# Performance work log

Measured on AMD Instinct MI355X. Metric: run time of the kernel, lower is better.

The kernel has to match this reference:

```python
import jax, jax.numpy as jnp
import numpy as np

H = 768
NH = 12
HD = H // NH
NDIM = 5
LN_EPS = 1e-5


def setup_inputs() -> dict:
    key = jax.random.key(0)
    ks = jax.random.split(key, 12)
    B, S = 4, 2048
    xavier = lambda k: jax.random.uniform(k, (H, H), jnp.float32, -1.0, 1.0) * np.sqrt(6.0 / (H + H))
    return {
        "hidden_states": jax.random.normal(ks[0], (B, S, H), jnp.float32),
        "Wq": xavier(ks[1]), "bq": jnp.zeros((H,), jnp.float32),
        "Wk": xavier(ks[2]), "bk": jnp.zeros((H,), jnp.float32),
        "Wv": xavier(ks[3]), "bv": jnp.zeros((H,), jnp.float32),
        "Wo": xavier(ks[4]), "bo": jnp.zeros((H,), jnp.float32),
        # per-dimension, per-head scalar biases (torch init: zeros; use small randn so grads are non-trivial)
        "dim_biases": 0.02 * jax.random.normal(ks[5], (NDIM, NH), jnp.float32),
        "ln_gamma": jnp.ones((H,), jnp.float32),
        "ln_beta": jnp.zeros((H,), jnp.float32),
        "attention_mask": jax.random.randint(ks[6], (4, 2048), 0, 2, jnp.int32),
        "dimension_idx": 2,
    }


def reference(hidden_states, Wq, bq, Wk, bk, Wv, bv, Wo, bo, dim_biases,
              ln_gamma, ln_beta, attention_mask, dimension_idx):
    B, S, _ = hidden_states.shape
    residual = hidden_states
    # torch nn.Linear: x @ W.T + b
    q = (hidden_states @ Wq.T + bq).reshape(B, S, NH, HD).transpose(0, 2, 1, 3)  # [B,NH,S,HD]
    k = (hidden_states @ Wk.T + bk).reshape(B, S, NH, HD).transpose(0, 2, 1, 3)
    v = (hidden_states @ Wv.T + bv).reshape(B, S, NH, HD).transpose(0, 2, 1, 3)

    scores = jnp.einsum("bhqd,bhkd->bhqk", q, k) / np.sqrt(HD)  # [B,NH,S,S]
    if dimension_idx is not None and dimension_idx < NDIM:
        scores = scores + dim_biases[dimension_idx][None, :, None, None]
    # mask over key positions, broadcast over heads and queries
    scores = jnp.where(attention_mask[:, None, None, :] == 0, -jnp.inf, scores)
    attn = jax.nn.softmax(scores, axis=-1)

    ctx = jnp.einsum("bhqk,bhkd->bhqd", attn, v)  # [B,NH,S,HD]
    ctx = ctx.transpose(0, 2, 1, 3).reshape(B, S, H)
    out = ctx @ Wo.T + bo

    y = out + residual
    mu = jnp.mean(y, axis=-1, keepdims=True)
    var = jnp.var(y, axis=-1, keepdims=True)
    y = (y - mu) / jnp.sqrt(var + LN_EPS) * ln_gamma + ln_beta
    return y
```

## Files before the change

### kernel.cpp

```cpp
#include <hip/hip_runtime.h>
#include <hip/hip_bf16.h>

#define HH    768
#define NHEAD 12
#define HDIM  64
#define BB    4
#define SS    2048
#define MM    (BB*SS)
#define NDIMS 5
#define WEL   (HH*HH)
#define LOG2E 1.44269504088896f
#define QSCALE 0.180336881f

typedef unsigned short u16;
typedef __attribute__((ext_vector_type(8))) short short8;
typedef __attribute__((ext_vector_type(4))) float floatx4;
typedef __attribute__((ext_vector_type(16))) float floatx16;
typedef __attribute__((ext_vector_type(4))) unsigned int uint4v;
typedef __attribute__((ext_vector_type(2))) unsigned int uint2v;

__device__ __forceinline__ float bf2f(u16 u) {
    return __uint_as_float(((unsigned int)u) << 16);
}
__device__ __forceinline__ u16 f2bf(float f) {
    unsigned int x = __float_as_uint(f);
    unsigned int r = (x + 0x7fffu + ((x >> 16) & 1u)) >> 16;
    return (u16)r;
}
__device__ __forceinline__ unsigned int pack_bf16x2(float a, float b) {
    float2 f2 = make_float2(a, b);
    __hip_bfloat162 h2 = __float22bfloat162_rn(f2);
    return *reinterpret_cast<unsigned int*>(&h2);
}
__device__ __forceinline__ void gld16(const u16* g, u16* l) {
    __builtin_amdgcn_global_load_lds(
        (const __attribute__((address_space(1))) unsigned int*)g,
        (__attribute__((address_space(3))) unsigned int*)l, 16, 0, 0);
}

__global__ __launch_bounds__(256) void f32_to_bf16(
    const float* __restrict__ in, u16* __restrict__ out, int n8)
{
    int i = blockIdx.x * 256 + threadIdx.x;
    if (i >= n8) return;
    float4 a = ((const float4*)in)[i*2];
    float4 b = ((const float4*)in)[i*2 + 1];
    ushort4 lo, hi;
    lo.x = f2bf(a.x); lo.y = f2bf(a.y); lo.z = f2bf(a.z); lo.w = f2bf(a.w);
    hi.x = f2bf(b.x); hi.y = f2bf(b.y); hi.z = f2bf(b.z); hi.w = f2bf(b.w);
    ((ushort4*)out)[i*2]     = lo;
    ((ushort4*)out)[i*2 + 1] = hi;
}

__global__ __launch_bounds__(256) void w_cvt4(
    const float* __restrict__ W0, const float* __restrict__ W1,
    const float* __restrict__ W2, const float* __restrict__ W3,
    u16* __restrict__ out)
{
    const float* src = (blockIdx.y == 0) ? W0 : (blockIdx.y == 1) ? W1
                     : (blockIdx.y == 2) ? W2 : W3;
    u16* dst = out + (size_t)blockIdx.y * WEL;
    int i = blockIdx.x * 256 + threadIdx.x;
    float4 a = ((const float4*)src)[i*2];
    float4 b = ((const float4*)src)[i*2 + 1];
    ushort4 lo, hi;
    lo.x = f2bf(a.x); lo.y = f2bf(a.y); lo.z = f2bf(a.z); lo.w = f2bf(a.w);
    hi.x = f2bf(b.x); hi.y = f2bf(b.y); hi.z = f2bf(b.z); hi.w = f2bf(b.w);
    ((ushort4*)dst)[i*2]     = lo;
    ((ushort4*)dst)[i*2 + 1] = hi;
}

__device__ __forceinline__ void gemm_gld_body(
    const u16* __restrict__ Xb, const u16* __restrict__ Wrows,
    const float* __restrict__ biasL, u16* __restrict__ outL, int i0)
{
    __shared__ u16 Xs[128][64];
    __shared__ u16 Ws[128][64];
    const int t = threadIdx.x;
    const int w = t >> 6, lane = t & 63;
    const int wy = w >> 1, wx = w & 1;
    const int m = lane & 31, hh = lane >> 5;

    const int grow = lane >> 3;
    const int cg   = (lane & 7) ^ grow;

    floatx16 acc[2][2];
    #pragma unroll
    for (int am = 0; am < 2; ++am)
        #pragma unroll
        for (int bn = 0; bn < 2; ++bn)
            #pragma unroll
            for (int r = 0; r < 16; ++r) acc[am][bn][r] = 0.f;

    for (int k0 = 0; k0 < HH; k0 += 64) {
        __syncthreads();
        #pragma unroll
        for (int j = 0; j < 4; ++j) {
            const int r = w*32 + j*8;
            gld16(Xb    + (size_t)(i0 + r + grow)*HH + k0 + cg*8, &Xs[r][0]);
            gld16(Wrows + (size_t)(r + grow)*HH      + k0 + cg*8, &Ws[r][0]);
        }
        __syncthreads();

        #pragma unroll
        for (int kh = 0; kh < 4; ++kh) {
            const int ch = kh*2 + hh;
            short8 af[2], bf[2];
            #pragma unroll
            for (int am = 0; am < 2; ++am) {
                const int row = wy*64 + am*32 + m;
                af[am] = *(const short8*)&Xs[row][(ch ^ (m & 7))*8];
            }
            #pragma unroll
            for (int bn = 0; bn < 2; ++bn) {
                const int row = wx*64 + bn*32 + m;
                bf[bn] = *(const short8*)&Ws[row][(ch ^ (m & 7))*8];
            }
            #pragma unroll
            for (int am = 0; am < 2; ++am)
                #pragma unroll
                for (int bn = 0; bn < 2; ++bn)
                    acc[am][bn] = __builtin_amdgcn_mfma_f32_32x32x16_bf16(
                        af[am], bf[bn], acc[am][bn], 0, 0, 0);
        }
    }

    float bb[2];
    #pragma unroll
    for (int bn = 0; bn < 2; ++bn) bb[bn] = biasL[wx*64 + bn*32 + m];
    #pragma unroll
    for (int am = 0; am < 2; ++am)
        #pragma unroll
        for (int bn = 0; bn < 2; ++bn)
            #pragma unroll
            for (int r = 0; r < 16; ++r) {
                int row = i0 + wy*64 + am*32 + (r & 3) + 8*(r >> 2) + 4*hh;
                outL[(size_t)row*HH + wx*64 + bn*32 + m] = f2bf(acc[am][bn][r] + bb[bn]);
            }
}

__global__ __launch_bounds__(256) void gemm_gld_qkv(
    const u16* __restrict__ Xb, const u16* __restrict__ Wb3,
    const float* __restrict__ bq, const float* __restrict__ bk, const float* __restrict__ bv,
    u16* __restrict__ oq, u16* __restrict__ ok, u16* __restrict__ ov)
{
    const int j0 = blockIdx.x * 128;
    const int sel = j0 / HH;
    const int lj = j0 - sel * HH;
    const float* bias = (sel == 0) ? bq : (sel == 1) ? bk : bv;
    u16* out = (sel == 0) ? oq : (sel == 1) ? ok : ov;
    gemm_gld_body(Xb, Wb3 + (size_t)j0 * HH, bias + lj, out + lj, blockIdx.y * 128);
}

__global__ __launch_bounds__(256) void gemm_gld_single(
    const u16* __restrict__ Xb, const u16* __restrict__ Wb,
    const float* __restrict__ bias, u16* __restrict__ out)
{
    const int j0 = blockIdx.x * 128;
    gemm_gld_body(Xb, Wb + (size_t)j0 * HH, bias + j0, out + j0, blockIdx.y * 128);
}

__global__ __launch_bounds__(256) void gemm_mfma_nt(
    const u16* __restrict__ Xb, const float* __restrict__ W,
    const float* __restrict__ bias, u16* __restrict__ out)
{
    __shared__ u16 Xs[128][40];
    __shared__ u16 Wt[64][40];
    const int t = threadIdx.x;
    const int w = t >> 6, lane = t & 63;
    const int c = lane & 15, qd = lane >> 4;
    const int i0 = blockIdx.y * 128, j0 = blockIdx.x * 64;
    const int xrow = t >> 1, xoff = (t & 1) * 16;
    const int wn = t >> 2, woff = (t & 3) * 8;

    floatx4 acc[2][4];
    #pragma unroll
    for (int mt = 0; mt < 2; ++mt)
        #pragma unroll
        for (int nt = 0; nt < 4; ++nt) acc[mt][nt] = (floatx4){0.f,0.f,0.f,0.f};

    for (int k0 = 0; k0 < HH; k0 += 32) {
        uint4 xa  = *(const uint4*)(Xb + (size_t)(i0 + xrow)*HH + k0 + xoff);
        uint4 xb2 = *(const uint4*)(Xb + (size_t)(i0 + xrow)*HH + k0 + xoff + 8);
        float4 wa = *(const float4*)(W + (size_t)(j0 + wn)*HH + k0 + woff);
        float4 wb = *(const float4*)(W + (size_t)(j0 + wn)*HH + k0 + woff + 4);
        __syncthreads();
        *(uint4*)&Xs[xrow][xoff]     = xa;
        *(uint4*)&Xs[xrow][xoff + 8] = xb2;
        ushort4 w0, w1;
        w0.x = f2bf(wa.x); w0.y = f2bf(wa.y); w0.z = f2bf(wa.z); w0.w = f2bf(wa.w);
        w1.x = f2bf(wb.x); w1.y = f2bf(wb.y); w1.z = f2bf(wb.z); w1.w = f2bf(wb.w);
        *(ushort4*)&Wt[wn][woff]     = w0;
        *(ushort4*)&Wt[wn][woff + 4] = w1;
        __syncthreads();

        short8 a0 = *(const short8*)&Xs[w*32 + c][qd*8];
        short8 a1 = *(const short8*)&Xs[w*32 + 16 + c][qd*8];
        #pragma unroll
        for (int nt = 0; nt < 4; ++nt) {
            short8 bfr = *(const short8*)&Wt[nt*16 + c][qd*8];
            acc[0][nt] = __builtin_amdgcn_mfma_f32_16x16x32_bf16(a0, bfr, acc[0][nt], 0, 0, 0);
            acc[1][nt] = __builtin_amdgcn_mfma_f32_16x16x32_bf16(a1, bfr, acc[1][nt], 0, 0, 0);
        }
    }

    float bv[4];
    #pragma unroll
    for (int nt = 0; nt < 4; ++nt) bv[nt] = bias[j0 + nt*16 + c];
    #pragma unroll
    for (int mt = 0; mt < 2; ++mt)
        #pragma unroll
        for (int nt = 0; nt < 4; ++nt)
            #pragma unroll
            for (int r = 0; r < 4; ++r)
                out[(size_t)(i0 + w*32 + mt*16 + qd*4 + r)*HH + j0 + nt*16 + c] =
                    f2bf(acc[mt][nt][r] + bv[nt]);
}

__global__ __launch_bounds__(256, 3) void attn_mfma32(
    const u16* __restrict__ Q, const u16* __restrict__ K, const u16* __restrict__ V,
    const float* __restrict__ dim_biases, const int* __restrict__ mask,
    const int* __restrict__ dim_idx_p, u16* __restrict__ ctx)
{
    __shared__ u16 Ks[2][64][64];
    __shared__ u16 Vt[2][64][64];
    __shared__ float madd[2][64];

    const int t = threadIdx.x;
    const int w = t >> 6, lane = t & 63;
    const int ql = lane & 31, hi = lane >> 5;
    const int sw7 = ql & 7;

    const int flat = blockIdx.x + 16 * (blockIdx.y + 12 * blockIdx.z);
    const int swz  = (flat & 7) * 96 + (flat >> 3);
    const int q0 = (swz & 15) * 128;
    const int h  = (swz >> 4) % NHEAD;
    const int b  = swz / (16 * NHEAD);

    const int didx = *dim_idx_p;
    const float db2 = ((didx < NDIMS) ? dim_biases[didx*NHEAD + h] : 0.f) * LOG2E;

    const int grow = lane >> 3;
    const int cg   = (lane & 7) ^ grow;
    const int vkp = t & 31;
    const int vdg = (t >> 5) * 8;

    short8 ones;
    #pragma unroll
    for (int j = 0; j < 8; ++j) ones[j] = (short)0x3F80;

    short8 qv[4];
    {
        const u16* qsrc = Q + ((size_t)(b*SS + q0 + w*32 + ql))*HH + h*HDIM + 8*hi;
        #pragma unroll
        for (int s = 0; s < 4; ++s) {
            ushort4 u0 = *(const ushort4*)(qsrc + s*16);
            ushort4 u1 = *(const ushort4*)(qsrc + s*16 + 4);
            const u16 uu[8] = {u0.x,u0.y,u0.z,u0.w,u1.x,u1.y,u1.z,u1.w};
            #pragma unroll
            for (int j = 0; j < 8; ++j)
                qv[s][j] = (short)f2bf(bf2f(uu[j]) * QSCALE);
        }
    }

    floatx16 o[2], lacc;
    #pragma unroll
    for (int r = 0; r < 16; ++r) { o[0][r] = 0.f; o[1][r] = 0.f; lacc[r] = 0.f; }

    auto stage = [&](int kt, int buf) {
        #pragma unroll
        for (int j = 0; j < 2; ++j) {
            const int rbase = w*16 + j*8;
            gld16(K + (size_t)(b*SS + kt*64 + rbase + grow)*HH + h*HDIM + cg*8,
                  &Ks[buf][rbase][0]);
        }
        const u16* va = V + ((size_t)(b*SS + kt*64 + 2*vkp))*HH + h*HDIM + vdg;
        const u16* vb = va + HH;
        ushort4 a0 = *(const ushort4*)va;
        ushort4 a1 = *(const ushort4*)(va + 4);
        ushort4 b0 = *(const ushort4*)vb;
        ushort4 b1 = *(const ushort4*)(vb + 4);
        const u16 aa[8] = {a0.x,a0.y,a0.z,a0.w,a1.x,a1.y,a1.z,a1.w};
        const u16 bb[8] = {b0.x,b0.y,b0.z,b0.w,b1.x,b1.y,b1.z,b1.w};
        #pragma unroll
        for (int i = 0; i < 8; ++i) {
            const int d = vdg + i;
            const int sc = (vkp >> 2) ^ (d & 7);
            *(unsigned int*)&Vt[buf][d][sc*8 + (vkp & 3)*2] =
                (unsigned int)aa[i] | ((unsigned int)bb[i] << 16);
        }
        if (t < 64)
            madd[buf][t] = (mask[(size_t)b*SS + kt*64 + t] != 0) ? db2 : -1e30f;
    };

    stage(0, 0);

    for (int kt = 0; kt < SS/64; ++kt) {
        const int cur = kt & 1;
        __syncthreads();
        if (kt + 1 < SS/64) stage(kt + 1, cur ^ 1);

        #pragma unroll
        for (int kblk = 0; kblk < 2; ++kblk) {
            const int krow = kblk*32 + ql;
            const u16* kb = &Ks[cur][krow][0];

            floatx16 z;
            #pragma unroll
            for (int qq = 0; qq < 4; ++qq) {
                float4 mv = *(const float4*)&madd[cur][kblk*32 + qq*8 + 4*hi];
                z[qq*4+0] = mv.x; z[qq*4+1] = mv.y; z[qq*4+2] = mv.z; z[qq*4+3] = mv.w;
            }
            #pragma unroll
            for (int s = 0; s < 4; ++s) {
                short8 kf = *(const short8*)(kb + ((s*2 + hi) ^ sw7)*8);
                z = __builtin_amdgcn_mfma_f32_32x32x16_bf16(kf, qv[s], z, 0, 0, 0);
            }
            #pragma unroll
            for (int r = 0; r < 16; ++r) z[r] = __builtin_amdgcn_exp2f(z[r]);

            #pragma unroll
            for (int ks = 0; ks < 2; ++ks) {
                unsigned x0 = pack_bf16x2(z[ks*8 + 0], z[ks*8 + 1]);
                unsigned y0 = pack_bf16x2(z[ks*8 + 4], z[ks*8 + 5]);
                unsigned x1 = pack_bf16x2(z[ks*8 + 2], z[ks*8 + 3]);
                unsigned y1 = pack_bf16x2(z[ks*8 + 6], z[ks*8 + 7]);
                uint2v s0 = __builtin_amdgcn_permlane32_swap(x0, y0, false, false);
                uint2v s1 = __builtin_amdgcn_permlane32_swap(x1, y1, false, false);
                uint4v pv; pv[0] = s0[0]; pv[1] = s1[0]; pv[2] = s0[1]; pv[3] = s1[1];
                short8 pa = __builtin_bit_cast(short8, pv);

                lacc = __builtin_amdgcn_mfma_f32_32x32x16_bf16(pa, ones, lacc, 0, 0, 0);
                const int ck = kblk*4 + ks*2 + hi;
                #pragma unroll
                for (int dblk = 0; dblk < 2; ++dblk) {
                    const int d = dblk*32 + ql;
                    short8 vf = *(const short8*)&Vt[cur][d][(ck ^ sw7)*8];
                    o[dblk] = __builtin_amdgcn_mfma_f32_32x32x16_bf16(pa, vf, o[dblk], 0, 0, 0);
                }
            }
        }
    }

    #pragma unroll
    for (int r = 0; r < 16; ++r) {
        float l = lacc[r];
        float inv = (l > 0.f) ? 1.f / l : 0.f;
        const int qrow = q0 + w*32 + (r & 3) + 8*(r >> 2) + 4*hi;
        u16* dst = ctx + ((size_t)(b*SS + qrow))*HH + h*HDIM + ql;
        dst[0]  = f2bf(o[0][r] * inv);
        dst[32] = f2bf(o[1][r] * inv);
    }
}

__global__ __launch_bounds__(256) void add_ln_wave(
    const u16* __restrict__ proj, const float* __restrict__ resid,
    const float* __restrict__ gamma, const float* __restrict__ beta,
    float* __restrict__ out)
{
    const int t = threadIdx.x, w = t >> 6, lane = t & 63;
    const int row = blockIdx.x * 4 + w;
    const size_t base = (size_t)row * HH + lane * 12;
    const int gbase = lane * 12;

    float x[12];
    #pragma unroll
    for (int j = 0; j < 3; ++j) {
        ushort4 p = *(const ushort4*)(proj + base + j*4);
        float4  r = *(const float4*)(resid + base + j*4);
        x[j*4+0] = bf2f(p.x) + r.x;
        x[j*4+1] = bf2f(p.y) + r.y;
        x[j*4+2] = bf2f(p.z) + r.z;
        x[j*4+3] = bf2f(p.w) + r.w;
    }
    float s = 0.f, ss = 0.f;
    #pragma unroll
    for (int j = 0; j < 12; ++j) { s += x[j]; ss += x[j]*x[j]; }
    #pragma unroll
    for (int off = 1; off < 64; off <<= 1) {
        s  += __shfl_xor(s, off);
        ss += __shfl_xor(ss, off);
    }
    float mean = s * (1.f/768.f);
    float var  = ss * (1.f/768.f) - mean*mean;
    float rstd = rsqrtf(fmaxf(var, 0.f) + 1e-5f);
    #pragma unroll
    for (int j = 0; j < 3; ++j) {
        float4 g = *(const float4*)(gamma + gbase + j*4);
        float4 bt = *(const float4*)(beta + gbase + j*4);
        float4 y;
        y.x = (x[j*4+0]-mean)*rstd*g.x + bt.x;
        y.y = (x[j*4+1]-mean)*rstd*g.y + bt.y;
        y.z = (x[j*4+2]-mean)*rstd*g.z + bt.z;
        y.w = (x[j*4+3]-mean)*rstd*g.w + bt.w;
        *(float4*)(out + base + j*4) = y;
    }
}

extern "C" void kernel_launch(void* const* d_in, const int* in_sizes, int n_in,
                              void* d_out, int out_size, void* d_ws, size_t ws_size,
                              hipStream_t stream)
{
    (void)in_sizes; (void)n_in; (void)out_size;
    const float* x    = (const float*)d_in[0];
    const float* Wq   = (const float*)d_in[1];
    const float* bq   = (const float*)d_in[2];
    const float* Wk   = (const float*)d_in[3];
    const float* bk   = (const float*)d_in[4];
    const float* Wv   = (const float*)d_in[5];
    const float* bv   = (const float*)d_in[6];
    const float* Wo   = (const float*)d_in[7];
    const float* bo   = (const float*)d_in[8];
    const float* dimb = (const float*)d_in[9];
    const float* gam  = (const float*)d_in[10];
    const float* bet  = (const float*)d_in[11];
    const int* mask   = (const int*)d_in[12];
    const int* didx   = (const int*)d_in[13];

    const size_t N = (size_t)MM * HH;
    if (ws_size < 4 * N * sizeof(u16)) return;
    u16* ws = (u16*)d_ws;
    u16* q    = ws;
    u16* kbuf = ws + N;
    u16* vbuf = ws + 2*N;
    u16* slot3 = ws + 3*N;
    u16* xb   = slot3;
    u16* ctx  = slot3;
    u16* proj = q;

    const bool bigws = ws_size >= (4 * N + 4 * (size_t)WEL) * sizeof(u16);
    u16* wb = ws + 4 * N;

    f32_to_bf16<<<(int)(N/8/256), 256, 0, stream>>>(x, xb, (int)(N/8));
    if (bigws) {
        w_cvt4<<<dim3(WEL/8/256, 4), 256, 0, stream>>>(Wq, Wk, Wv, Wo, wb);
        gemm_gld_qkv<<<dim3(3*HH/128, MM/128), 256, 0, stream>>>(
            xb, wb, bq, bk, bv, q, kbuf, vbuf);
    } else {
        dim3 gg(HH/64, MM/128);
        gemm_mfma_nt<<<gg, 256, 0, stream>>>(xb, Wq, bq, q);
        gemm_mfma_nt<<<gg, 256, 0, stream>>>(xb, Wk, bk, kbuf);
        gemm_mfma_nt<<<gg, 256, 0, stream>>>(xb, Wv, bv, vbuf);
    }
    attn_mfma32<<<dim3(SS/128, NHEAD, BB), 256, 0, stream>>>(q, kbuf, vbuf, dimb, mask, didx, ctx);
    if (bigws) gemm_gld_single<<<dim3(HH/128, MM/128), 256, 0, stream>>>(ctx, wb + 3*WEL, bo, proj);
    else {
        dim3 gg(HH/64, MM/128);
        gemm_mfma_nt<<<gg, 256, 0, stream>>>(ctx, Wo, bo, proj);
    }
    add_ln_wave<<<MM/4, 256, 0, stream>>>(proj, x, gam, bet, (float*)d_out);
}
```

Before: 260.1 us.

## Process two 32-row query groups per wave to reuse K/V fragments

Each attention wave now handles 64 query rows as two 32-row groups, so every K and V fragment read from LDS feeds two MFMAs. The block query tile grows from 128 to 256 and the grid is halved, with the swizzle remapped to match. MFMA sections are wrapped in s_setprio, and K fragments are hoisted into registers before the MFMA chain. This lowers LDS traffic and K/V staging per unit of work, but raises register pressure (occupancy hint lowered from 3 to 2) and leaves only 384 blocks to fill the GPU.

```diff
diff --git a/kernel.cpp b/kernel.cpp
--- a/kernel.cpp
+++ b/kernel.cpp
@@ -217,7 +217,7 @@
                     f2bf(acc[mt][nt][r] + bv[nt]);
 }
 
-__global__ __launch_bounds__(256, 3) void attn_mfma32(
+__global__ __launch_bounds__(256, 2) void attn_mfma32(
     const u16* __restrict__ Q, const u16* __restrict__ K, const u16* __restrict__ V,
     const float* __restrict__ dim_biases, const int* __restrict__ mask,
     const int* __restrict__ dim_idx_p, u16* __restrict__ ctx)
@@ -231,11 +231,11 @@
     const int ql = lane & 31, hi = lane >> 5;
     const int sw7 = ql & 7;
 
-    const int flat = blockIdx.x + 16 * (blockIdx.y + 12 * blockIdx.z);
-    const int swz  = (flat & 7) * 96 + (flat >> 3);
-    const int q0 = (swz & 15) * 128;
-    const int h  = (swz >> 4) % NHEAD;
-    const int b  = swz / (16 * NHEAD);
+    const int flat = blockIdx.x + 8 * (blockIdx.y + 12 * blockIdx.z);
+    const int swz  = (flat & 7) * 48 + (flat >> 3);
+    const int q0 = (swz & 7) * 256;
+    const int h  = (swz >> 3) % NHEAD;
+    const int b  = swz / (8 * NHEAD);
 
     const int didx = *dim_idx_p;
     const float db2 = ((didx < NDIMS) ? dim_biases[didx*NHEAD + h] : 0.f) * LOG2E;
@@ -249,9 +249,10 @@
     #pragma unroll
     for (int j = 0; j < 8; ++j) ones[j] = (short)0x3F80;
 
-    short8 qv[4];
-    {
-        const u16* qsrc = Q + ((size_t)(b*SS + q0 + w*32 + ql))*HH + h*HDIM + 8*hi;
+    short8 qv[2][4];
+    #pragma unroll
+    for (int g = 0; g < 2; ++g) {
+        const u16* qsrc = Q + ((size_t)(b*SS + q0 + w*64 + g*32 + ql))*HH + h*HDIM + 8*hi;
         #pragma unroll
         for (int s = 0; s < 4; ++s) {
             ushort4 u0 = *(const ushort4*)(qsrc + s*16);
@@ -259,13 +260,17 @@
             const u16 uu[8] = {u0.x,u0.y,u0.z,u0.w,u1.x,u1.y,u1.z,u1.w};
             #pragma unroll
             for (int j = 0; j < 8; ++j)
-                qv[s][j] = (short)f2bf(bf2f(uu[j]) * QSCALE);
-        }
-    }
-
-    floatx16 o[2], lacc;
-    #pragma unroll
-    for (int r = 0; r < 16; ++r) { o[0][r] = 0.f; o[1][r] = 0.f; lacc[r] = 0.f; }
+                qv[g][s][j] = (short)f2bf(bf2f(uu[j]) * QSCALE);
+        }
+    }
+
+    floatx16 o[2][2], lacc[2];
+    #pragma unroll
+    for (int r = 0; r < 16; ++r) {
+        o[0][0][r] = 0.f; o[0][1][r] = 0.f;
+        o[1][0][r] = 0.f; o[1][1][r] = 0.f;
+        lacc[0][r] = 0.f; lacc[1][r] = 0.f;
+    }
 
     auto stage = [&](int kt, int buf) {
         #pragma unroll
@@ -305,51 +310,81 @@
             const int krow = kblk*32 + ql;
             const u16* kb = &Ks[cur][krow][0];
 
-            floatx16 z;
+            floatx16 z0, z1;
             #pragma unroll
             for (int qq = 0; qq < 4; ++qq) {
                 float4 mv = *(const float4*)&madd[cur][kblk*32 + qq*8 + 4*hi];
-                z[qq*4+0] = mv.x; z[qq*4+1] = mv.y; z[qq*4+2] = mv.z; z[qq*4+3] = mv.w;
-            }
+                z0[qq*4+0] = mv.x; z0[qq*4+1] = mv.y; z0[qq*4+2] = mv.z; z0[qq*4+3] = mv.w;
+                z1[qq*4+0] = mv.x; z1[qq*4+1] = mv.y; z1[qq*4+2] = mv.z; z1[qq*4+3] = mv.w;
+            }
+            short8 kf[4];
+            #pragma unroll
+            for (int s = 0; s < 4; ++s)
+                kf[s] = *(const short8*)(kb + ((s*2 + hi) ^ sw7)*8);
+            __builtin_amdgcn_s_setprio(1);
             #pragma unroll
             for (int s = 0; s < 4; ++s) {
-                short8 kf = *(const short8*)(kb + ((s*2 + hi) ^ sw7)*8);
-                z = __builtin_amdgcn_mfma_f32_32x32x16_bf16(kf, qv[s], z, 0, 0, 0);
-            }
-            #pragma unroll
-            for (int r = 0; r < 16; ++r) z[r] = __builtin_amdgcn_exp2f(z[r]);
+                z0 = __builtin_amdgcn_mfma_f32_32x32x16_bf16(kf[s], qv[0][s], z0, 0, 0, 0);
+                z1 = __builtin_amdgcn_mfma_f32_32x32x16_bf16(kf[s], qv[1][s], z1, 0, 0, 0);
+            }
+            __builtin_amdgcn_s_setprio(0);
+
+            #pragma unroll
+            for (int r = 0; r < 16; ++r) {
+                z0[r] = __builtin_amdgcn_exp2f(z0[r]);
+                z1[r] = __builtin_amdgcn_exp2f(z1[r]);
+            }
 
             #pragma unroll
             for (int ks = 0; ks < 2; ++ks) {
-                unsigned x0 = pack_bf16x2(z[ks*8 + 0], z[ks*8 + 1]);
-                unsigned y0 = pack_bf16x2(z[ks*8 + 4], z[ks*8 + 5]);
-                unsigned x1 = pack_bf16x2(z[ks*8 + 2], z[ks*8 + 3]);
-                unsigned y1 = pack_bf16x2(z[ks*8 + 6], z[ks*8 + 7]);
-                uint2v s0 = __builtin_amdgcn_permlane32_swap(x0, y0, false, false);
-                uint2v s1 = __builtin_amdgcn_permlane32_swap(x1, y1, false, false);
-                uint4v pv; pv[0] = s0[0]; pv[1] = s1[0]; pv[2] = s0[1]; pv[3] = s1[1];
-                short8 pa = __builtin_bit_cast(short8, pv);
-
-                lacc = __builtin_amdgcn_mfma_f32_32x32x16_bf16(pa, ones, lacc, 0, 0, 0);
+                unsigned x00 = pack_bf16x2(z0[ks*8 + 0], z0[ks*8 + 1]);
+                unsigned y00 = pack_bf16x2(z0[ks*8 + 4], z0[ks*8 + 5]);
+                unsigned x01 = pack_bf16x2(z0[ks*8 + 2], z0[ks*8 + 3]);
+                unsigned y01 = pack_bf16x2(z0[ks*8 + 6], z0[ks*8 + 7]);
+                uint2v s00 = __builtin_amdgcn_permlane32_swap(x00, y00, false, false);
+                uint2v s01 = __builtin_amdgcn_permlane32_swap(x01, y01, false, false);
+                uint4v pv0; pv0[0] = s00[0]; pv0[1] = s01[0]; pv0[2] = s00[1]; pv0[3] = s01[1];
+                short8 pa0 = __builtin_bit_cast(short8, pv0);
+
+                unsigned x10 = pack_bf16x2(z1[ks*8 + 0], z1[ks*8 + 1]);
+                unsigned y10 = pack_bf16x2(z1[ks*8 + 4], z1[ks*8 + 5]);
+                unsigned x11 = pack_bf16x2(z1[ks*8 + 2], z1[ks*8 + 3]);
+                unsigned y11 = pack_bf16x2(z1[ks*8 + 6], z1[ks*8 + 7]);
+                uint2v s10 = __builtin_amdgcn_permlane32_swap(x10, y10, false, false);
+                uint2v s11 = __builtin_amdgcn_permlane32_swap(x11, y11, false, false);
+                uint4v pv1; pv1[0] = s10[0]; pv1[1] = s11[0]; pv1[2] = s10[1]; pv1[3] = s11[1];
+                short8 pa1 = __builtin_bit_cast(short8, pv1);
+
                 const int ck = kblk*4 + ks*2 + hi;
+                short8 vf[2];
+                #pragma unroll
+                for (int dblk = 0; dblk < 2; ++dblk)
+                    vf[dblk] = *(const short8*)&Vt[cur][dblk*32 + ql][(ck ^ sw7)*8];
+
+                __builtin_amdgcn_s_setprio(1);
+                lacc[0] = __builtin_amdgcn_mfma_f32_32x32x16_bf16(pa0, ones, lacc[0], 0, 0, 0);
+                lacc[1] = __builtin_amdgcn_mfma_f32_32x32x16_bf16(pa1, ones, lacc[1], 0, 0, 0);
                 #pragma unroll
                 for (int dblk = 0; dblk < 2; ++dblk) {
-                    const int d = dblk*32 + ql;
-                    short8 vf = *(const short8*)&Vt[cur][d][(ck ^ sw7)*8];
-                    o[dblk] = __builtin_amdgcn_mfma_f32_32x32x16_bf16(pa, vf, o[dblk], 0, 0, 0);
+                    o[0][dblk] = __builtin_amdgcn_mfma_f32_32x32x16_bf16(pa0, vf[dblk], o[0][dblk], 0, 0, 0);
+                    o[1][dblk] = __builtin_amdgcn_mfma_f32_32x32x16_bf16(pa1, vf[dblk], o[1][dblk], 0, 0, 0);
                 }
-            }
-        }
-    }
-
-    #pragma unroll
-    for (int r = 0; r < 16; ++r) {
-        float l = lacc[r];
-        float inv = (l > 0.f) ? 1.f / l : 0.f;
-        const int qrow = q0 + w*32 + (r & 3) + 8*(r >> 2) + 4*hi;
-        u16* dst = ctx + ((size_t)(b*SS + qrow))*HH + h*HDIM + ql;
-        dst[0]  = f2bf(o[0][r] * inv);
-        dst[32] = f2bf(o[1][r] * inv);
+                __builtin_amdgcn_s_setprio(0);
+            }
+        }
+    }
+
+    #pragma unroll
+    for (int g = 0; g < 2; ++g) {
+        #pragma unroll
+        for (int r = 0; r < 16; ++r) {
+            float l = lacc[g][r];
+            float inv = (l > 0.f) ? 1.f / l : 0.f;
+            const int qrow = q0 + w*64 + g*32 + (r & 3) + 8*(r >> 2) + 4*hi;
+            u16* dst = ctx + ((size_t)(b*SS + qrow))*HH + h*HDIM + ql;
+            dst[0]  = f2bf(o[g][0][r] * inv);
+            dst[32] = f2bf(o[g][1][r] * inv);
+        }
     }
 }
 
@@ -442,7 +477,7 @@
         gemm_mfma_nt<<<gg, 256, 0, stream>>>(xb, Wk, bk, kbuf);
         gemm_mfma_nt<<<gg, 256, 0, stream>>>(xb, Wv, bv, vbuf);
     }
-    attn_mfma32<<<dim3(SS/128, NHEAD, BB), 256, 0, stream>>>(q, kbuf, vbuf, dimb, mask, didx, ctx);
+    attn_mfma32<<<dim3(SS/256, NHEAD, BB), 256, 0, stream>>>(q, kbuf, vbuf, dimb, mask, didx, ctx);
     if (bigws) gemm_gld_single<<<dim3(HH/128, MM/128), 256, 0, stream>>>(ctx, wb + 3*WEL, bo, proj);
     else {
         dim3 gg(HH/64, MM/128);
```

Result: slower. 268.7 us (+3.3%).

## Defer V transpose writes past compute, pad Vt, add setprio, merge conversion kernels

Applied to the files above, without the earlier changes.

In the attention kernel, the next tile's global V and mask loads are issued into registers before compute, and their transposed LDS writes happen after the current tile's MFMAs. This hides global load latency behind the matrix work. The V tile now uses a padded row stride instead of an XOR swizzle. K fragments are preloaded before the MFMA chains, which are wrapped in s_setprio. The activation and four weight f32→bf16 conversions are merged into one launch to cut launch overhead, at the cost of extra registers held across the loop.

```diff
diff --git a/kernel.cpp b/kernel.cpp
--- a/kernel.cpp
+++ b/kernel.cpp
@@ -14,6 +14,7 @@
 
 typedef unsigned short u16;
 typedef __attribute__((ext_vector_type(8))) short short8;
+typedef __attribute__((ext_vector_type(4))) short short4v;
 typedef __attribute__((ext_vector_type(4))) float floatx4;
 typedef __attribute__((ext_vector_type(16))) float floatx16;
 typedef __attribute__((ext_vector_type(4))) unsigned int uint4v;
@@ -52,15 +53,26 @@
     ((ushort4*)out)[i*2 + 1] = hi;
 }
 
-__global__ __launch_bounds__(256) void w_cvt4(
+#define XCVT_BLKS ((MM*HH)/8/256)
+#define WCVT_BLKS (WEL/8/256)
+__global__ __launch_bounds__(256) void cvt_all(
+    const float* __restrict__ x,
     const float* __restrict__ W0, const float* __restrict__ W1,
     const float* __restrict__ W2, const float* __restrict__ W3,
-    u16* __restrict__ out)
-{
-    const float* src = (blockIdx.y == 0) ? W0 : (blockIdx.y == 1) ? W1
-                     : (blockIdx.y == 2) ? W2 : W3;
-    u16* dst = out + (size_t)blockIdx.y * WEL;
-    int i = blockIdx.x * 256 + threadIdx.x;
+    u16* __restrict__ xb, u16* __restrict__ wb)
+{
+    const int bid = blockIdx.x;
+    const float* src;
+    u16* dst;
+    int i;
+    if (bid < XCVT_BLKS) {
+        src = x; dst = xb; i = bid * 256 + threadIdx.x;
+    } else {
+        const int wsel = (bid - XCVT_BLKS) / WCVT_BLKS;
+        src = (wsel == 0) ? W0 : (wsel == 1) ? W1 : (wsel == 2) ? W2 : W3;
+        dst = wb + (size_t)wsel * WEL;
+        i = ((bid - XCVT_BLKS) % WCVT_BLKS) * 256 + threadIdx.x;
+    }
     float4 a = ((const float4*)src)[i*2];
     float4 b = ((const float4*)src)[i*2 + 1];
     ushort4 lo, hi;
@@ -223,7 +235,7 @@
     const int* __restrict__ dim_idx_p, u16* __restrict__ ctx)
 {
     __shared__ u16 Ks[2][64][64];
-    __shared__ u16 Vt[2][64][64];
+    __shared__ u16 Vt[2][64][68];
     __shared__ float madd[2][64];
 
     const int t = threadIdx.x;
@@ -267,43 +279,48 @@
     #pragma unroll
     for (int r = 0; r < 16; ++r) { o[0][r] = 0.f; o[1][r] = 0.f; lacc[r] = 0.f; }
 
-    auto stage = [&](int kt, int buf) {
+    uint4 VA, VB;
+    int mreg = 0;
+
+    auto issueK = [&](int kt, int buf) {
         #pragma unroll
         for (int j = 0; j < 2; ++j) {
             const int rbase = w*16 + j*8;
             gld16(K + (size_t)(b*SS + kt*64 + rbase + grow)*HH + h*HDIM + cg*8,
                   &Ks[buf][rbase][0]);
         }
+    };
+    auto issueV = [&](int kt) {
         const u16* va = V + ((size_t)(b*SS + kt*64 + 2*vkp))*HH + h*HDIM + vdg;
-        const u16* vb = va + HH;
-        ushort4 a0 = *(const ushort4*)va;
-        ushort4 a1 = *(const ushort4*)(va + 4);
-        ushort4 b0 = *(const ushort4*)vb;
-        ushort4 b1 = *(const ushort4*)(vb + 4);
-        const u16 aa[8] = {a0.x,a0.y,a0.z,a0.w,a1.x,a1.y,a1.z,a1.w};
-        const u16 bb[8] = {b0.x,b0.y,b0.z,b0.w,b1.x,b1.y,b1.z,b1.w};
-        #pragma unroll
-        for (int i = 0; i < 8; ++i) {
-            const int d = vdg + i;
-            const int sc = (vkp >> 2) ^ (d & 7);
-            *(unsigned int*)&Vt[buf][d][sc*8 + (vkp & 3)*2] =
-                (unsigned int)aa[i] | ((unsigned int)bb[i] << 16);
-        }
-        if (t < 64)
-            madd[buf][t] = (mask[(size_t)b*SS + kt*64 + t] != 0) ? db2 : -1e30f;
+        VA = *(const uint4*)va;
+        VB = *(const uint4*)(va + HH);
+        if (t < 64) mreg = mask[(size_t)b*SS + kt*64 + t];
     };
-
-    stage(0, 0);
+    auto writeV = [&](int buf) {
+        const unsigned* Aw = (const unsigned*)&VA;
+        const unsigned* Bw = (const unsigned*)&VB;
+        #pragma unroll
+        for (int i2 = 0; i2 < 4; ++i2) {
+            unsigned a = Aw[i2], bb = Bw[i2];
+            *(unsigned*)&Vt[buf][vdg + 2*i2][2*vkp]     = (a & 0xffffu) | (bb << 16);
+            *(unsigned*)&Vt[buf][vdg + 2*i2 + 1][2*vkp] = (a >> 16) | (bb & 0xffff0000u);
+        }
+        if (t < 64) madd[buf][t] = (mreg != 0) ? db2 : -1e30f;
+    };
+
+    issueK(0, 0);
+    issueV(0);
+    writeV(0);
 
     for (int kt = 0; kt < SS/64; ++kt) {
         const int cur = kt & 1;
         __syncthreads();
-        if (kt + 1 < SS/64) stage(kt + 1, cur ^ 1);
+        const bool more = (kt + 1 < SS/64);
+        if (more) { issueK(kt + 1, cur ^ 1); issueV(kt + 1); }
 
         #pragma unroll
         for (int kblk = 0; kblk < 2; ++kblk) {
-            const int krow = kblk*32 + ql;
-            const u16* kb = &Ks[cur][krow][0];
+            const u16* kb = &Ks[cur][kblk*32 + ql][0];
 
             floatx16 z;
             #pragma unroll
@@ -311,11 +328,16 @@
                 float4 mv = *(const float4*)&madd[cur][kblk*32 + qq*8 + 4*hi];
                 z[qq*4+0] = mv.x; z[qq*4+1] = mv.y; z[qq*4+2] = mv.z; z[qq*4+3] = mv.w;
             }
-            #pragma unroll
-            for (int s = 0; s < 4; ++s) {
-                short8 kf = *(const short8*)(kb + ((s*2 + hi) ^ sw7)*8);
-                z = __builtin_amdgcn_mfma_f32_32x32x16_bf16(kf, qv[s], z, 0, 0, 0);
-            }
+            short8 kf[4];
+            #pragma unroll
+            for (int s = 0; s < 4; ++s)
+                kf[s] = *(const short8*)(kb + ((s*2 + hi) ^ sw7)*8);
+            __builtin_amdgcn_s_setprio(1);
+            #pragma unroll
+            for (int s = 0; s < 4; ++s)
+                z = __builtin_amdgcn_mfma_f32_32x32x16_bf16(kf[s], qv[s], z, 0, 0, 0);
+            __builtin_amdgcn_s_setprio(0);
+
             #pragma unroll
             for (int r = 0; r < 16; ++r) z[r] = __builtin_amdgcn_exp2f(z[r]);
 
@@ -330,16 +352,29 @@
                 uint4v pv; pv[0] = s0[0]; pv[1] = s1[0]; pv[2] = s0[1]; pv[3] = s1[1];
                 short8 pa = __builtin_bit_cast(short8, pv);
 
+                const int ck = kblk*4 + ks*2 + hi;
+                const u16* vp0 = &Vt[cur][ql][ck*8];
+                const u16* vp1 = &Vt[cur][32 + ql][ck*8];
+                short4v a0 = *(const short4v*)vp0;
+                short4v a1 = *(const short4v*)(vp0 + 4);
+                short4v b0 = *(const short4v*)vp1;
+                short4v b1 = *(const short4v*)(vp1 + 4);
+                short8 vf0, vf1;
+                #pragma unroll
+                for (int j = 0; j < 4; ++j) {
+                    vf0[j] = a0[j]; vf0[4+j] = a1[j];
+                    vf1[j] = b0[j]; vf1[4+j] = b1[j];
+                }
+
+                __builtin_amdgcn_s_setprio(1);
                 lacc = __builtin_amdgcn_mfma_f32_32x32x16_bf16(pa, ones, lacc, 0, 0, 0);
-                const int ck = kblk*4 + ks*2 + hi;
-                #pragma unroll
-                for (int dblk = 0; dblk < 2; ++dblk) {
-                    const int d = dblk*32 + ql;
-                    short8 vf = *(const short8*)&Vt[cur][d][(ck ^ sw7)*8];
-                    o[dblk] = __builtin_amdgcn_mfma_f32_32x32x16_bf16(pa, vf, o[dblk], 0, 0, 0);
-                }
+                o[0] = __builtin_amdgcn_mfma_f32_32x32x16_bf16(pa, vf0, o[0], 0, 0, 0);
+                o[1] = __builtin_amdgcn_mfma_f32_32x32x16_bf16(pa, vf1, o[1], 0, 0, 0);
+                __builtin_amdgcn_s_setprio(0);
             }
         }
+
+        if (more) writeV(cur ^ 1);
     }
 
     #pragma unroll
@@ -431,12 +466,12 @@
     const bool bigws = ws_size >= (4 * N + 4 * (size_t)WEL) * sizeof(u16);
     u16* wb = ws + 4 * N;
 
-    f32_to_bf16<<<(int)(N/8/256), 256, 0, stream>>>(x, xb, (int)(N/8));
     if (bigws) {
-        w_cvt4<<<dim3(WEL/8/256, 4), 256, 0, stream>>>(Wq, Wk, Wv, Wo, wb);
+        cvt_all<<<XCVT_BLKS + 4*WCVT_BLKS, 256, 0, stream>>>(x, Wq, Wk, Wv, Wo, xb, wb);
         gemm_gld_qkv<<<dim3(3*HH/128, MM/128), 256, 0, stream>>>(
             xb, wb, bq, bk, bv, q, kbuf, vbuf);
     } else {
+        f32_to_bf16<<<(int)(N/8/256), 256, 0, stream>>>(x, xb, (int)(N/8));
         dim3 gg(HH/64, MM/128);
         gemm_mfma_nt<<<gg, 256, 0, stream>>>(xb, Wq, bq, q);
         gemm_mfma_nt<<<gg, 256, 0, stream>>>(xb, Wk, bk, kbuf);
```

Measured after the change: 245.6 us. 1.06x faster.
